# Optimization experiments

Measured on AMD Instinct MI355X. Metric: run time of the kernel, lower is better.

## Reference

```python
import jax, jax.numpy as jnp
import numpy as np

N = 100000; EI = 1600000; EC = 800000; G = 2000
FD = 512; H1 = 32; H2 = 32; EMB = 128; NH = 4
EPS = 1e-5


def setup_inputs() -> dict:
    key = jax.random.key(0)
    ks = jax.random.split(key, 30)
    p = lambda k, shp: (jax.random.normal(k, shp, jnp.float32) * 0.05)
    inp = {
        'feat': jax.random.normal(ks[0], (N, FD), jnp.float32),
        'inter_src': jax.random.randint(ks[1], (EI,), 0, N),
        'inter_dst': jax.random.randint(ks[2], (EI,), 0, N),
        'cross_src': jax.random.randint(ks[3], (EC,), 0, N),
        'cross_dst': jax.random.randint(ks[4], (EC,), 0, N),
        'graph_ids': jnp.sort(jax.random.randint(ks[5], (N,), 0, G)),
        # layer1
        'W_gc1': p(ks[6], (FD, NH * H1)), 'b_gc1': p(ks[7], (NH * H1,)),
        'W_gat1': p(ks[8], (FD, NH * H1)), 'al1': p(ks[9], (NH, H1)), 'ar1': p(ks[10], (NH, H1)), 'b_gat1': p(ks[11], (NH * H1,)),
        # layer2
        'W_gc2': p(ks[12], (NH * H1, NH * H2)), 'b_gc2': p(ks[13], (NH * H2,)),
        'W_gat2': p(ks[14], (NH * H1, NH * H2)), 'al2': p(ks[15], (NH, H2)), 'ar2': p(ks[16], (NH, H2)), 'b_gat2': p(ks[17], (NH * H2,)),
        # layer3
        'W_gc3': p(ks[18], (NH * H2, EMB)), 'b_gc3': p(ks[19], (EMB,)),
        'W_gat3': p(ks[20], (NH * H2, EMB)), 'al3': p(ks[21], (1, EMB)), 'ar3': p(ks[22], (1, EMB)), 'b_gat3': p(ks[23], (EMB,)),
        # batchnorms (gamma ones, beta zeros)
        'g1': jnp.ones((NH * H1,), jnp.float32), 'be1': jnp.zeros((NH * H1,), jnp.float32),
        'g2': jnp.ones((NH * H2,), jnp.float32), 'be2': jnp.zeros((NH * H2,), jnp.float32),
        'g3': jnp.ones((EMB,), jnp.float32), 'be3': jnp.zeros((EMB,), jnp.float32),
    }
    return inp


def _leaky(x):
    return jnp.where(x >= 0, x, 0.2 * x)


def _graph_conv(x, W, b, src, dst):
    # DGL GraphConv, norm='both': D_out^{-1/2} A D_in^{-1/2} X W + b (degrees clamped to >=1)
    ones = jnp.ones(src.shape[0], x.dtype)
    dout = jnp.clip(jax.ops.segment_sum(ones, src, num_segments=N), 1.0)
    din = jnp.clip(jax.ops.segment_sum(ones, dst, num_segments=N), 1.0)
    xw = (x @ W) * (dout ** -0.5)[:, None]          # project first (in >= out)
    agg = jax.ops.segment_sum(xw[src], dst, num_segments=N)
    return agg * (din ** -0.5)[:, None] + b


def _gat(x, W, al, ar, b, src, dst, H, d):
    # DGL GATConv: per-edge additive attention with edge softmax over incoming edges
    f = (x @ W).reshape(-1, H, d)                    # [N,H,d]
    el = jnp.sum(f * al, -1)                         # [N,H]
    er = jnp.sum(f * ar, -1)
    e = _leaky(el[src] + er[dst])                    # [E,H]
    m = jax.ops.segment_max(e, dst, num_segments=N)
    ex = jnp.exp(e - m[dst])
    s = jax.ops.segment_sum(ex, dst, num_segments=N)
    alpha = ex / s[dst]                              # [E,H]
    out = jax.ops.segment_sum(alpha[:, :, None] * f[src], dst, num_segments=N)
    return out + b.reshape(1, H, d), alpha


def _bn(x, g, b):
    mu = x.mean(0)
    v = jnp.mean((x - mu) ** 2, 0)
    return g * (x - mu) / jnp.sqrt(v + EPS) + b


def reference(feat, inter_src, inter_dst, cross_src, cross_dst, graph_ids,
              W_gc1, b_gc1, W_gat1, al1, ar1, b_gat1,
              W_gc2, b_gc2, W_gat2, al2, ar2, b_gat2,
              W_gc3, b_gc3, W_gat3, al3, ar3, b_gat3,
              g1, be1, g2, be2, g3, be3):
    h = feat
    hi = _graph_conv(h, W_gc1, b_gc1, inter_src, inter_dst)
    hc, _ = _gat(h, W_gat1, al1, ar1, b_gat1, cross_src, cross_dst, NH, H1)
    h = _bn(_leaky(hi + hc.reshape(N, -1)), g1, be1)
    hi = _graph_conv(h, W_gc2, b_gc2, inter_src, inter_dst)
    hc, _ = _gat(h, W_gat2, al2, ar2, b_gat2, cross_src, cross_dst, NH, H2)
    h = _bn(_leaky(hi + hc.reshape(N, -1)), g2, be2)
    h1 = _graph_conv(h, W_gc3, b_gc3, inter_src, inter_dst)
    h2, att = _gat(h, W_gat3, al3, ar3, b_gat3, cross_src, cross_dst, 1, EMB)
    h = _bn(h1 + h2[:, 0, :], g3, be3)
    att_sum = jax.ops.segment_sum(att[:, 0], cross_src, num_segments=N)   # [N]
    wh = h * att_sum[:, None]
    gsum = jax.ops.segment_sum(wh, graph_ids, num_segments=G)
    cnt = jnp.clip(jax.ops.segment_sum(jnp.ones(N, h.dtype), graph_ids, num_segments=G), 1.0)
    frag_embeddings = gsum / cnt[:, None]                                  # [G,EMB]
    return frag_embeddings, att_sum
```

## Files before the change

### kernel.cpp

```cpp
#include <hip/hip_runtime.h>
#include <math.h>

#define NN 100000
#define EIE 1600000
#define ECE 800000
#define GG 2000
#define FDIM 512
#define CC 128
#define BNEPS 1e-5f
#define SLOTI 48
#define SLOTC 32
#define FUSED_BLOCKS 3910

static inline int cdiv(long a, long b){ return (int)((a+b-1)/b); }

typedef __attribute__((ext_vector_type(8))) short short8;
typedef __attribute__((ext_vector_type(4))) float f32x4;

__device__ __forceinline__ unsigned short f2bf(float f){
  unsigned u = __float_as_uint(f);
  u += 0x7fffu + ((u >> 16) & 1u);
  return (unsigned short)(u >> 16);
}
__device__ __forceinline__ float bf2f(unsigned short h){
  return __uint_as_float(((unsigned)h) << 16);
}
__device__ __forceinline__ float2 ldbf2(const unsigned short* p){
  ushort2 u = *(const ushort2*)p;
  return make_float2(bf2f(u.x), bf2f(u.y));
}

__device__ __forceinline__ size_t wt_off(int n, int k) {
  return (size_t)(k >> 5)*8192 + (((n >> 4)*4 + ((k >> 3) & 3))*16 + (n & 15))*8 + (k & 7);
}
__global__ void k_pack_all(const float* __restrict__ Wgc1, const float* __restrict__ Wgat1,
                           const float* __restrict__ Wgc2, const float* __restrict__ Wgat2,
                           const float* __restrict__ Wgc3, const float* __restrict__ Wgat3,
                           unsigned short* __restrict__ Wth1, unsigned short* __restrict__ Wtl1,
                           unsigned short* __restrict__ Wth2, unsigned short* __restrict__ Wtl2,
                           unsigned short* __restrict__ Wth3, unsigned short* __restrict__ Wtl3) {
  int t = blockIdx.x*256 + threadIdx.x;
  const float *W1, *W2; unsigned short *oh, *ol; int FIN, tt;
  if (t < 131072)      { W1=Wgc1; W2=Wgat1; oh=Wth1; ol=Wtl1; FIN=512; tt=t; }
  else if (t < 163840) { W1=Wgc2; W2=Wgat2; oh=Wth2; ol=Wtl2; FIN=128; tt=t-131072; }
  else if (t < 196608) { W1=Wgc3; W2=Wgat3; oh=Wth3; ol=Wtl3; FIN=128; tt=t-163840; }
  else return;
  int n = tt / FIN, k = tt % FIN;
  float v = (n < 128) ? W1[(size_t)k*128 + n] : W2[(size_t)k*128 + (n-128)];
  unsigned short h = f2bf(v);
  size_t o = wt_off(n, k);
  oh[o] = h;
  ol[o] = f2bf(v - bf2f(h));
}

__global__ __launch_bounds__(512)
void k_fill_gemm1(const int* __restrict__ isrc, const int* __restrict__ idst,
                  const int* __restrict__ csrc, const int* __restrict__ cdst,
                  int* __restrict__ cnt_i, int* __restrict__ eid_i,
                  int* __restrict__ cnt_c, int* __restrict__ eid_c,
                  int* __restrict__ dout, float* __restrict__ att,
                  const float* __restrict__ xf,
                  const unsigned short* __restrict__ Bh, const unsigned short* __restrict__ Bl,
                  const float* __restrict__ al, const float* __restrict__ ar,
                  float* __restrict__ el, float* __restrict__ er,
                  unsigned short* __restrict__ Y1, unsigned short* __restrict__ Y2) {
  __shared__ __attribute__((aligned(16))) unsigned short sAh[4096];
  __shared__ __attribute__((aligned(16))) unsigned short sBh[8192];
  __shared__ __attribute__((aligned(16))) unsigned short sBl[8192];
  int r = blockIdx.x;
  int tid = threadIdx.x;

  if (r % 5 != 0) {
    int fi = r - 1 - (r-1)/5;
    int e = fi*512 + tid;
    if (e < EIE) {
      int d = idst[e];
      int p = atomicAdd(&cnt_i[d], 1);
      if (p < SLOTI) eid_i[d*SLOTI + p] = isrc[e];
      atomicAdd(&dout[isrc[e]], 1);
    }
    if (e < ECE) {
      int d = cdst[e];
      int p = atomicAdd(&cnt_c[d], 1);
      if (p < SLOTC) eid_c[d*SLOTC + p] = csrc[e];
    }
    if (e < NN) att[e] = 0.f;
    return;
  }

  int row0 = (r/5)*128;
  int lane = tid & 63, wid = tid >> 6;
  int wm = wid >> 2, wn = wid & 3;
  int l15 = lane & 15, quad = lane >> 4;

  f32x4 acc[4][4];
  #pragma unroll
  for (int mt = 0; mt < 4; ++mt)
    #pragma unroll
    for (int nt = 0; nt < 4; ++nt) acc[mt][nt] = (f32x4){0.f,0.f,0.f,0.f};

  for (int k0 = 0; k0 < FDIM; k0 += 32) {
    #pragma unroll
    for (int i = 0; i < 2; ++i) {
      int idx = tid + i*512;
      int rr = idx >> 3, c = idx & 7;
      int gr = row0 + rr; if (gr > NN-1) gr = NN-1;
      float4 v = *(const float4*)(xf + (size_t)gr*FDIM + k0 + c*4);
      ushort4 hh;
      hh.x = f2bf(v.x); hh.y = f2bf(v.y); hh.z = f2bf(v.z); hh.w = f2bf(v.w);
      *(ushort4*)&sAh[(((rr>>4)*4 + (c>>1))*16 + (rr&15))*8 + (c&1)*4] = hh;
    }
    const unsigned short* bhk = Bh + (size_t)k0*256;
    const unsigned short* blk = Bl + (size_t)k0*256;
    #pragma unroll
    for (int i = 0; i < 2; ++i) {
      int idx = tid + i*512;
      *(float4*)&sBh[idx*8] = *(const float4*)(bhk + idx*8);
      *(float4*)&sBl[idx*8] = *(const float4*)(blk + idx*8);
    }
    __syncthreads();
    short8 ah[4];
    #pragma unroll
    for (int mt = 0; mt < 4; ++mt)
      ah[mt] = *(const short8*)&sAh[(((wm*4+mt)*4 + quad)*16 + l15)*8];
    #pragma unroll
    for (int nt = 0; nt < 4; ++nt) {
      int off = (((wn*4+nt)*4 + quad)*16 + l15)*8;
      short8 bh = *(const short8*)&sBh[off];
      short8 bl = *(const short8*)&sBl[off];
      #pragma unroll
      for (int mt = 0; mt < 4; ++mt) {
        acc[mt][nt] = __builtin_amdgcn_mfma_f32_16x16x32_bf16(ah[mt], bh, acc[mt][nt], 0,0,0);
        acc[mt][nt] = __builtin_amdgcn_mfma_f32_16x16x32_bf16(ah[mt], bl, acc[mt][nt], 0,0,0);
      }
    }
    __syncthreads();
  }
  unsigned short* Y = (wn < 2) ? Y1 : Y2;
  int colbase = (wn & 1)*64;
  #pragma unroll
  for (int mt = 0; mt < 4; ++mt) {
    #pragma unroll
    for (int rr = 0; rr < 4; ++rr) {
      int row = row0 + (wm*4+mt)*16 + quad*4 + rr;
      if (row >= NN) continue;
      #pragma unroll
      for (int nt = 0; nt < 4; ++nt)
        Y[(size_t)row*CC + colbase + nt*16 + l15] = f2bf(acc[mt][nt][rr]);
    }
  }
  if (wn >= 2) {
    float alv[4], arv[4];
    #pragma unroll
    for (int nt = 0; nt < 4; ++nt) {
      int col = colbase + nt*16 + l15;
      alv[nt] = al[col]; arv[nt] = ar[col];
    }
    int hb = (wn & 1)*2;
    #pragma unroll
    for (int mt = 0; mt < 4; ++mt) {
      #pragma unroll
      for (int rr = 0; rr < 4; ++rr) {
        float pa0 = acc[mt][0][rr]*alv[0] + acc[mt][1][rr]*alv[1];
        float pb0 = acc[mt][0][rr]*arv[0] + acc[mt][1][rr]*arv[1];
        float pa1 = acc[mt][2][rr]*alv[2] + acc[mt][3][rr]*alv[3];
        float pb1 = acc[mt][2][rr]*arv[2] + acc[mt][3][rr]*arv[3];
        #pragma unroll
        for (int m = 1; m <= 8; m <<= 1) {
          pa0 += __shfl_xor(pa0, m); pb0 += __shfl_xor(pb0, m);
          pa1 += __shfl_xor(pa1, m); pb1 += __shfl_xor(pb1, m);
        }
        int row = row0 + (wm*4+mt)*16 + quad*4 + rr;
        if (l15 == 0 && row < NN) {
          el[(size_t)row*4 + hb]   = pa0;  er[(size_t)row*4 + hb]   = pb0;
          el[(size_t)row*4 + hb+1] = pa1;  er[(size_t)row*4 + hb+1] = pb1;
        }
      }
    }
  }
}

template<bool ELR4, bool ELR1>
__global__ __launch_bounds__(512)
void k_gemm2(const unsigned short* __restrict__ xb,
             const unsigned short* __restrict__ Bh, const unsigned short* __restrict__ Bl,
             const float* __restrict__ csqin, const float* __restrict__ g,
             const float* __restrict__ be, const int* __restrict__ dout,
             const float* __restrict__ al, const float* __restrict__ ar,
             float* __restrict__ el, float* __restrict__ er,
             unsigned short* __restrict__ Y1, unsigned short* __restrict__ Y2) {
  __shared__ __attribute__((aligned(16))) unsigned short sAh[4096];
  __shared__ __attribute__((aligned(16))) unsigned short sBh[8192];
  __shared__ __attribute__((aligned(16))) unsigned short sBl[8192];
  __shared__ float sSC[CC], sSH[CC];
  int tid = threadIdx.x;
  int row0 = blockIdx.x*128;
  int lane = tid & 63, wid = tid >> 6;
  int wm = wid >> 2, wn = wid & 3;
  int l15 = lane & 15, quad = lane >> 4;

  if (tid < CC) {
    float sv = csqin[tid], qv = csqin[CC + tid];
    float mu = sv * (1.f/NN);
    float var = qv * (1.f/NN) - mu*mu;
    float rn = rsqrtf(var + BNEPS);
    float s = g[tid]*rn;
    sSC[tid] = s;
    sSH[tid] = be[tid] - s*mu;
  }
  __syncthreads();

  f32x4 acc[4][4];
  #pragma unroll
  for (int mt = 0; mt < 4; ++mt)
    #pragma unroll
    for (int nt = 0; nt < 4; ++nt) acc[mt][nt] = (f32x4){0.f,0.f,0.f,0.f};

  for (int k0 = 0; k0 < CC; k0 += 32) {
    int rr = tid >> 2, c16 = tid & 3;
    int gr = row0 + rr; if (gr > NN-1) gr = NN-1;
    short8 u = *(const short8*)(xb + (size_t)gr*CC + k0 + c16*8);
    short8 o;
    #pragma unroll
    for (int j = 0; j < 8; ++j) {
      float f = bf2f((unsigned short)u[j]);
      f = f*sSC[k0 + c16*8 + j] + sSH[k0 + c16*8 + j];
      o[j] = (short)f2bf(f);
    }
    *(short8*)&sAh[(((rr>>4)*4 + c16)*16 + (rr&15))*8] = o;

    const unsigned short* bhk = Bh + (size_t)k0*256;
    const unsigned short* blk = Bl + (size_t)k0*256;
    #pragma unroll
    for (int i = 0; i < 2; ++i) {
      int idx = tid + i*512;
      *(float4*)&sBh[idx*8] = *(const float4*)(bhk + idx*8);
      *(float4*)&sBl[idx*8] = *(const float4*)(blk + idx*8);
    }
    __syncthreads();
    short8 ah[4];
    #pragma unroll
    for (int mt = 0; mt < 4; ++mt)
      ah[mt] = *(const short8*)&sAh[(((wm*4+mt)*4 + quad)*16 + l15)*8];
    #pragma unroll
    for (int nt = 0; nt < 4; ++nt) {
      int off = (((wn*4+nt)*4 + quad)*16 + l15)*8;
      short8 bh = *(const short8*)&sBh[off];
      short8 bl = *(const short8*)&sBl[off];
      #pragma unroll
      for (int mt = 0; mt < 4; ++mt) {
        acc[mt][nt] = __builtin_amdgcn_mfma_f32_16x16x32_bf16(ah[mt], bh, acc[mt][nt], 0,0,0);
        acc[mt][nt] = __builtin_amdgcn_mfma_f32_16x16x32_bf16(ah[mt], bl, acc[mt][nt], 0,0,0);
      }
    }
    __syncthreads();
  }
  unsigned short* Y = (wn < 2) ? Y1 : Y2;
  int colbase = (wn & 1)*64;
  #pragma unroll
  for (int mt = 0; mt < 4; ++mt) {
    #pragma unroll
    for (int rr = 0; rr < 4; ++rr) {
      int row = row0 + (wm*4+mt)*16 + quad*4 + rr;
      if (row >= NN) continue;
      float scv = (wn < 2) ? rsqrtf((float)max(dout[row], 1)) : 1.0f;
      #pragma unroll
      for (int nt = 0; nt < 4; ++nt)
        Y[(size_t)row*CC + colbase + nt*16 + l15] = f2bf(acc[mt][nt][rr]*scv);
    }
  }
  if constexpr (ELR4) {
    if (wn >= 2) {
      float alv[4], arv[4];
      #pragma unroll
      for (int nt = 0; nt < 4; ++nt) {
        int col = colbase + nt*16 + l15;
        alv[nt] = al[col]; arv[nt] = ar[col];
      }
      int hb = (wn & 1)*2;
      #pragma unroll
      for (int mt = 0; mt < 4; ++mt) {
        #pragma unroll
        for (int rr = 0; rr < 4; ++rr) {
          float pa0 = acc[mt][0][rr]*alv[0] + acc[mt][1][rr]*alv[1];
          float pb0 = acc[mt][0][rr]*arv[0] + acc[mt][1][rr]*arv[1];
          float pa1 = acc[mt][2][rr]*alv[2] + acc[mt][3][rr]*alv[3];
          float pb1 = acc[mt][2][rr]*arv[2] + acc[mt][3][rr]*arv[3];
          #pragma unroll
          for (int m = 1; m <= 8; m <<= 1) {
            pa0 += __shfl_xor(pa0, m); pb0 += __shfl_xor(pb0, m);
            pa1 += __shfl_xor(pa1, m); pb1 += __shfl_xor(pb1, m);
          }
          int row = row0 + (wm*4+mt)*16 + quad*4 + rr;
          if (l15 == 0 && row < NN) {
            el[(size_t)row*4 + hb]   = pa0;  er[(size_t)row*4 + hb]   = pb0;
            el[(size_t)row*4 + hb+1] = pa1;  er[(size_t)row*4 + hb+1] = pb1;
          }
        }
      }
    }
  }
  if constexpr (ELR1) {
    __shared__ float sE[2][2][CC];
    if (wn >= 2) {
      float alv[4], arv[4];
      #pragma unroll
      for (int nt = 0; nt < 4; ++nt) {
        int col = colbase + nt*16 + l15;
        alv[nt] = al[col]; arv[nt] = ar[col];
      }
      #pragma unroll
      for (int mt = 0; mt < 4; ++mt) {
        #pragma unroll
        for (int rr = 0; rr < 4; ++rr) {
          float pa = acc[mt][0][rr]*alv[0] + acc[mt][1][rr]*alv[1]
                   + acc[mt][2][rr]*alv[2] + acc[mt][3][rr]*alv[3];
          float pb = acc[mt][0][rr]*arv[0] + acc[mt][1][rr]*arv[1]
                   + acc[mt][2][rr]*arv[2] + acc[mt][3][rr]*arv[3];
          #pragma unroll
          for (int m = 1; m <= 8; m <<= 1) {
            pa += __shfl_xor(pa, m); pb += __shfl_xor(pb, m);
          }
          int rowl = (wm*4+mt)*16 + quad*4 + rr;
          if (l15 == 0) { sE[0][wn-2][rowl] = pa; sE[1][wn-2][rowl] = pb; }
        }
      }
    }
    __syncthreads();
    if (tid < CC) {
      int row = row0 + tid;
      if (row < NN) {
        el[row] = sE[0][0][tid] + sE[0][1][tid];
        er[row] = sE[1][0][tid] + sE[1][1][tid];
      }
    }
  }
}

template<int H, bool DSC, bool ATT, bool LEAKY>
__global__ __launch_bounds__(64)
void k_gather_fused(const unsigned short* __restrict__ A1, const unsigned short* __restrict__ A2,
                    const int* __restrict__ cnt_i, const int* __restrict__ eid_i,
                    const int* __restrict__ cnt_c, const int* __restrict__ eid_c,
                    const int* __restrict__ dout,
                    const float* __restrict__ el, const float* __restrict__ er,
                    const float* __restrict__ bgc, const float* __restrict__ bgat,
                    unsigned short* __restrict__ out, float* __restrict__ att) {
  int lane = threadIdx.x;
  int row = blockIdx.x;
  int grp = lane >> 4;
  int l4  = lane & 15;
  int c8  = l4*8;

  int deg = cnt_i[row];
  int lo = row*SLOTI, hi = lo + min(deg, SLOTI);
  float ax[8];
  #pragma unroll
  for (int k = 0; k < 8; ++k) ax[k] = 0.f;
  int j = lo + grp;
  for (; j + 4 < hi; j += 8) {
    int s0 = eid_i[j], s1 = eid_i[j+4];
    float d0 = DSC ? rsqrtf((float)max(dout[s0], 1)) : 1.0f;
    float d1 = DSC ? rsqrtf((float)max(dout[s1], 1)) : 1.0f;
    short8 u0 = *(const short8*)(A1 + (size_t)s0*CC + c8);
    short8 u1 = *(const short8*)(A1 + (size_t)s1*CC + c8);
    #pragma unroll
    for (int k = 0; k < 8; ++k) {
      if (DSC) ax[k] += d0*bf2f((unsigned short)u0[k]) + d1*bf2f((unsigned short)u1[k]);
      else     ax[k] += bf2f((unsigned short)u0[k]) + bf2f((unsigned short)u1[k]);
    }
  }
  if (j < hi) {
    int s0 = eid_i[j];
    float d0 = DSC ? rsqrtf((float)max(dout[s0], 1)) : 1.0f;
    short8 u0 = *(const short8*)(A1 + (size_t)s0*CC + c8);
    #pragma unroll
    for (int k = 0; k < 8; ++k) {
      if (DSC) ax[k] += d0*bf2f((unsigned short)u0[k]);
      else     ax[k] += bf2f((unsigned short)u0[k]);
    }
  }
  float sc = rsqrtf((float)max(deg, 1));

  int h = (H == 1) ? 0 : (l4 >> 2);
  float erd = er[(size_t)row*H + h];
  int degc = cnt_c[row];
  int lo2 = row*SLOTC, hi2 = lo2 + min(degc, SLOTC);
  float gacc[8];
  #pragma unroll
  for (int k = 0; k < 8; ++k) gacc[k] = 0.f;
  float denom = 0.f;
  j = lo2 + grp;
  for (; j + 4 < hi2; j += 8) {
    int s0 = eid_c[j], s1 = eid_c[j+4];
    float v0 = el[(size_t)s0*H + h] + erd;
    float v1 = el[(size_t)s1*H + h] + erd;
    v0 = (v0 >= 0.f) ? v0 : 0.2f*v0;
    v1 = (v1 >= 0.f) ? v1 : 0.2f*v1;
    float w0 = __expf(v0), w1 = __expf(v1);
    denom += w0 + w1;
    short8 u0 = *(const short8*)(A2 + (size_t)s0*CC + c8);
    short8 u1 = *(const short8*)(A2 + (size_t)s1*CC + c8);
    #pragma unroll
    for (int k = 0; k < 8; ++k)
      gacc[k] += w0*bf2f((unsigned short)u0[k]) + w1*bf2f((unsigned short)u1[k]);
  }
  if (j < hi2) {
    int s = eid_c[j];
    float v = el[(size_t)s*H + h] + erd;
    v = (v >= 0.f) ? v : 0.2f*v;
    float w = __expf(v);
    denom += w;
    short8 u = *(const short8*)(A2 + (size_t)s*CC + c8);
    #pragma unroll
    for (int k = 0; k < 8; ++k) gacc[k] += w * bf2f((unsigned short)u[k]);
  }

  #pragma unroll
  for (int m = 16; m <= 32; m <<= 1) {
    denom += __shfl_xor(denom, m);
    #pragma unroll
    for (int k = 0; k < 8; ++k) {
      ax[k]   += __shfl_xor(ax[k], m);
      gacc[k] += __shfl_xor(gacc[k], m);
    }
  }
  float inv = (denom > 0.f) ? 1.0f/denom : 0.f;

  if (ATT) {
    for (j = lo2 + grp; j < hi2; j += 4) {
      int s = eid_c[j];
      if (l4 == 0) {
        float v = el[(size_t)s*H] + erd;
        v = (v >= 0.f) ? v : 0.2f*v;
        atomicAdd(&att[s], __expf(v)*inv);
      }
    }
  }

  if (grp == 0) {
    float4 b1a = *(const float4*)(bgc + c8);
    float4 b1b = *(const float4*)(bgc + c8 + 4);
    float4 b2a = *(const float4*)(bgat + c8);
    float4 b2b = *(const float4*)(bgat + c8 + 4);
    float bb1[8] = {b1a.x,b1a.y,b1a.z,b1a.w,b1b.x,b1b.y,b1b.z,b1b.w};
    float bb2[8] = {b2a.x,b2a.y,b2a.z,b2a.w,b2b.x,b2b.y,b2b.z,b2b.w};
    short8 ov;
    #pragma unroll
    for (int k = 0; k < 8; ++k) {
      float o = ax[k]*sc + bb1[k] + gacc[k]*inv + bb2[k];
      if (LEAKY) o = (o >= 0.f) ? o : 0.2f*o;
      ov[k] = (short)f2bf(o);
    }
    *(short8*)(out + (size_t)row*CC + c8) = ov;
  }
}

__global__ __launch_bounds__(256)
void k_bn_stats(const unsigned short* __restrict__ t, float* __restrict__ csq) {
  __shared__ float red[4][128];
  int lane = threadIdx.x & 63, g = threadIdx.x >> 6;
  int c2 = lane*2;
  float s0=0.f, s1=0.f, q0=0.f, q1=0.f;
  for (int r = blockIdx.x*4 + g; r < NN; r += gridDim.x*4) {
    float2 v = ldbf2(t + (size_t)r*CC + c2);
    s0 += v.x; s1 += v.y; q0 += v.x*v.x; q1 += v.y*v.y;
  }
  red[g][c2] = s0; red[g][c2+1] = s1;
  __syncthreads();
  if (threadIdx.x < 128) {
    float a = red[0][threadIdx.x] + red[1][threadIdx.x] + red[2][threadIdx.x] + red[3][threadIdx.x];
    atomicAdd(&csq[threadIdx.x], a);
  }
  __syncthreads();
  red[g][c2] = q0; red[g][c2+1] = q1;
  __syncthreads();
  if (threadIdx.x < 128) {
    float a = red[0][threadIdx.x] + red[1][threadIdx.x] + red[2][threadIdx.x] + red[3][threadIdx.x];
    atomicAdd(&csq[128 + threadIdx.x], a);
  }
}

__global__ void k_bn_coef(const float* __restrict__ csqc,
                          const float* __restrict__ g, const float* __restrict__ be,
                          float* __restrict__ sc, float* __restrict__ sh) {
  int c = threadIdx.x;
  float mu = csqc[c] * (1.f/NN);
  float var = csqc[128+c] * (1.f/NN) - mu*mu;
  float r = rsqrtf(var + BNEPS);
  float s = g[c]*r;
  sc[c] = s;
  sh[c] = be[c] - s*mu;
}

__global__ void k_pool_bn(const unsigned short* __restrict__ t, const float* __restrict__ att,
                          const int* __restrict__ gids, const float* __restrict__ bnsc,
                          const float* __restrict__ bnsh, float* __restrict__ frag) {
  int g = blockIdx.x;
  __shared__ int se[2];
  if (threadIdx.x < 2) {
    int target = g + threadIdx.x;
    int lo = 0, hi = NN;
    while (lo < hi) { int mid = (lo + hi) >> 1; if (gids[mid] < target) lo = mid + 1; else hi = mid; }
    se[threadIdx.x] = lo;
  }
  __syncthreads();
  int lo = se[0], hi = se[1];
  int col = threadIdx.x;
  float scv = bnsc[col], shv = bnsh[col];
  float acc = 0.f;
  for (int n = lo; n < hi; ++n) acc += (bf2f(t[(size_t)n*CC + col])*scv + shv) * att[n];
  frag[(size_t)g*CC + col] = acc / (float)max(hi - lo, 1);
}

extern "C" void kernel_launch(void* const* d_in, const int* in_sizes, int n_in,
                              void* d_out, int out_size, void* d_ws, size_t ws_size,
                              hipStream_t stream) {
  const float* feat  = (const float*)d_in[0];
  const int* isrc    = (const int*)d_in[1];
  const int* idst    = (const int*)d_in[2];
  const int* csrc    = (const int*)d_in[3];
  const int* cdst    = (const int*)d_in[4];
  const int* gids    = (const int*)d_in[5];
  const float* W_gc1 = (const float*)d_in[6];  const float* b_gc1 = (const float*)d_in[7];
  const float* W_gat1= (const float*)d_in[8];  const float* al1   = (const float*)d_in[9];
  const float* ar1   = (const float*)d_in[10]; const float* b_gat1= (const float*)d_in[11];
  const float* W_gc2 = (const float*)d_in[12]; const float* b_gc2 = (const float*)d_in[13];
  const float* W_gat2= (const float*)d_in[14]; const float* al2   = (const float*)d_in[15];
  const float* ar2   = (const float*)d_in[16]; const float* b_gat2= (const float*)d_in[17];
  const float* W_gc3 = (const float*)d_in[18]; const float* b_gc3 = (const float*)d_in[19];
  const float* W_gat3= (const float*)d_in[20]; const float* al3   = (const float*)d_in[21];
  const float* ar3   = (const float*)d_in[22]; const float* b_gat3= (const float*)d_in[23];
  const float* g1 = (const float*)d_in[24]; const float* be1 = (const float*)d_in[25];
  const float* g2 = (const float*)d_in[26]; const float* be2 = (const float*)d_in[27];
  const float* g3 = (const float*)d_in[28]; const float* be3 = (const float*)d_in[29];

  const size_t NC = (size_t)NN*CC;
  float* el   = (float*)d_ws;
  float* er   = el + (size_t)NN*4;
  float* csq  = er + (size_t)NN*4;
  float* bnsc = csq + 768;
  float* bnsh = bnsc + CC;
  unsigned short* B  = (unsigned short*)(bnsh + CC);
  unsigned short* A1 = B + NC;
  unsigned short* A2 = A1 + NC;
  unsigned short* Wth1 = A2 + NC;
  unsigned short* Wtl1 = Wth1 + 256*FDIM;
  unsigned short* Wth2 = Wtl1 + 256*FDIM;
  unsigned short* Wtl2 = Wth2 + 256*CC;
  unsigned short* Wth3 = Wtl2 + 256*CC;
  unsigned short* Wtl3 = Wth3 + 256*CC;
  int* cnt_i  = (int*)(Wtl3 + 256*CC);
  int* cnt_c  = cnt_i + NN;
  int* dout   = cnt_c + NN;
  int* eid_i  = dout + NN;
  int* eid_c  = eid_i + (size_t)NN*SLOTI;

  float* frag = (float*)d_out;
  float* att  = frag + (size_t)GG*CC;

  hipMemsetAsync(cnt_i, 0, 3*(size_t)NN*sizeof(int), stream);
  hipMemsetAsync(csq, 0, 768*sizeof(float), stream);
  k_pack_all<<<cdiv(196608,256), 256, 0, stream>>>(W_gc1, W_gat1, W_gc2, W_gat2, W_gc3, W_gat3,
                                                   Wth1, Wtl1, Wth2, Wtl2, Wth3, Wtl3);
  k_fill_gemm1<<<FUSED_BLOCKS, 512, 0, stream>>>(isrc, idst, csrc, cdst,
                                                 cnt_i, eid_i, cnt_c, eid_c, dout, att,
                                                 feat, Wth1, Wtl1, al1, ar1, el, er, A1, A2);

  k_gather_fused<4,true,false,true><<<NN, 64, 0, stream>>>(A1, A2, cnt_i, eid_i,
                                                           cnt_c, eid_c, dout, el, er,
                                                           b_gc1, b_gat1, B, nullptr);
  k_bn_stats<<<256, 256, 0, stream>>>(B, csq);

  k_gemm2<true,false><<<cdiv(NN,128), 512, 0, stream>>>(B, Wth2, Wtl2, csq, g1, be1, dout,
                                                        al2, ar2, el, er, A1, A2);
  k_gather_fused<4,false,false,true><<<NN, 64, 0, stream>>>(A1, A2, cnt_i, eid_i,
                                                            cnt_c, eid_c, dout, el, er,
                                                            b_gc2, b_gat2, B, nullptr);
  k_bn_stats<<<256, 256, 0, stream>>>(B, csq + 256);

  k_gemm2<false,true><<<cdiv(NN,128), 512, 0, stream>>>(B, Wth3, Wtl3, csq + 256, g2, be2, dout,
                                                        al3, ar3, el, er, A1, A2);
  k_gather_fused<1,false,true,false><<<NN, 64, 0, stream>>>(A1, A2, cnt_i, eid_i,
                                                            cnt_c, eid_c, dout, el, er,
                                                            b_gc3, b_gat3, B, att);
  k_bn_stats<<<256, 256, 0, stream>>>(B, csq + 512);
  k_bn_coef<<<1, 128, 0, stream>>>(csq + 512, g3, be3, bnsc, bnsh);

  k_pool_bn<<<GG, 128, 0, stream>>>(B, att, gids, bnsc, bnsh, frag);
}
```

Baseline: 997.7 us.

## Fuse batchnorm statistics into persistent gather kernel with per-wave partials

The gather kernel becomes a grid-stride persistent kernel: 8192 waves, two per 128-thread block, each loop over many rows. Each wave accumulates per-channel sum and sum of squares of its fp32 outputs and writes them to a partials buffer. A small reduction kernel then folds the partials into the stats buffer, replacing the separate pass that re-read the bf16 output. This removes one full read of the activations per layer and the per-row block launch overhead, but adds a partials buffer and computes stats on pre-rounding fp32 values rather than the stored bf16 ones.

```diff
diff --git a/kernel.cpp b/kernel.cpp
--- a/kernel.cpp
+++ b/kernel.cpp
@@ -11,6 +11,8 @@
 #define SLOTI 48
 #define SLOTC 32
 #define FUSED_BLOCKS 3910
+#define GWG 4096
+#define NWAVES 8192
 
 static inline int cdiv(long a, long b){ return (int)((a+b-1)/b); }
 
@@ -338,147 +340,152 @@
 }
 
 template<int H, bool DSC, bool ATT, bool LEAKY>
-__global__ __launch_bounds__(64)
+__global__ __launch_bounds__(128)
 void k_gather_fused(const unsigned short* __restrict__ A1, const unsigned short* __restrict__ A2,
                     const int* __restrict__ cnt_i, const int* __restrict__ eid_i,
                     const int* __restrict__ cnt_c, const int* __restrict__ eid_c,
                     const int* __restrict__ dout,
                     const float* __restrict__ el, const float* __restrict__ er,
                     const float* __restrict__ bgc, const float* __restrict__ bgat,
-                    unsigned short* __restrict__ out, float* __restrict__ att) {
-  int lane = threadIdx.x;
-  int row = blockIdx.x;
+                    unsigned short* __restrict__ out, float* __restrict__ att,
+                    float* __restrict__ partial) {
+  int lane = threadIdx.x & 63;
+  int wave = blockIdx.x*2 + (threadIdx.x >> 6);
   int grp = lane >> 4;
   int l4  = lane & 15;
   int c8  = l4*8;
 
-  int deg = cnt_i[row];
-  int lo = row*SLOTI, hi = lo + min(deg, SLOTI);
-  float ax[8];
-  #pragma unroll
-  for (int k = 0; k < 8; ++k) ax[k] = 0.f;
-  int j = lo + grp;
-  for (; j + 4 < hi; j += 8) {
-    int s0 = eid_i[j], s1 = eid_i[j+4];
-    float d0 = DSC ? rsqrtf((float)max(dout[s0], 1)) : 1.0f;
-    float d1 = DSC ? rsqrtf((float)max(dout[s1], 1)) : 1.0f;
-    short8 u0 = *(const short8*)(A1 + (size_t)s0*CC + c8);
-    short8 u1 = *(const short8*)(A1 + (size_t)s1*CC + c8);
+  float bb1[8], bb2[8];
+  {
+    float4 a = *(const float4*)(bgc + c8);
+    float4 b = *(const float4*)(bgc + c8 + 4);
+    float4 c = *(const float4*)(bgat + c8);
+    float4 d = *(const float4*)(bgat + c8 + 4);
+    bb1[0]=a.x; bb1[1]=a.y; bb1[2]=a.z; bb1[3]=a.w;
+    bb1[4]=b.x; bb1[5]=b.y; bb1[6]=b.z; bb1[7]=b.w;
+    bb2[0]=c.x; bb2[1]=c.y; bb2[2]=c.z; bb2[3]=c.w;
+    bb2[4]=d.x; bb2[5]=d.y; bb2[6]=d.z; bb2[7]=d.w;
+  }
+  float s2x = 0.f, s2y = 0.f, q2x = 0.f, q2y = 0.f;
+
+  for (int row = wave; row < NN; row += NWAVES) {
+    int deg = cnt_i[row];
+    int lo = row*SLOTI, hi = lo + min(deg, SLOTI);
+    float ax[8];
+    #pragma unroll
+    for (int k = 0; k < 8; ++k) ax[k] = 0.f;
+    int j = lo + grp;
+    for (; j + 4 < hi; j += 8) {
+      int s0 = eid_i[j], s1 = eid_i[j+4];
+      float d0 = DSC ? rsqrtf((float)max(dout[s0], 1)) : 1.0f;
+      float d1 = DSC ? rsqrtf((float)max(dout[s1], 1)) : 1.0f;
+      short8 u0 = *(const short8*)(A1 + (size_t)s0*CC + c8);
+      short8 u1 = *(const short8*)(A1 + (size_t)s1*CC + c8);
+      #pragma unroll
+      for (int k = 0; k < 8; ++k) {
+        if (DSC) ax[k] += d0*bf2f((unsigned short)u0[k]) + d1*bf2f((unsigned short)u1[k]);
+        else     ax[k] += bf2f((unsigned short)u0[k]) + bf2f((unsigned short)u1[k]);
+      }
+    }
+    if (j < hi) {
+      int s0 = eid_i[j];
+      float d0 = DSC ? rsqrtf((float)max(dout[s0], 1)) : 1.0f;
+      short8 u0 = *(const short8*)(A1 + (size_t)s0*CC + c8);
+      #pragma unroll
+      for (int k = 0; k < 8; ++k) {
+        if (DSC) ax[k] += d0*bf2f((unsigned short)u0[k]);
+        else     ax[k] += bf2f((unsigned short)u0[k]);
+      }
+    }
+    float sc = rsqrtf((float)max(deg, 1));
+
+    int h = (H == 1) ? 0 : (l4 >> 2);
+    float erd = er[(size_t)row*H + h];
+    int degc = cnt_c[row];
+    int lo2 = row*SLOTC, hi2 = lo2 + min(degc, SLOTC);
+    float gacc[8];
+    #pragma unroll
+    for (int k = 0; k < 8; ++k) gacc[k] = 0.f;
+    float denom = 0.f;
+    j = lo2 + grp;
+    for (; j + 4 < hi2; j += 8) {
+      int s0 = eid_c[j], s1 = eid_c[j+4];
+      float v0 = el[(size_t)s0*H + h] + erd;
+      float v1 = el[(size_t)s1*H + h] + erd;
+      v0 = (v0 >= 0.f) ? v0 : 0.2f*v0;
+      v1 = (v1 >= 0.f) ? v1 : 0.2f*v1;
+      float w0 = __expf(v0), w1 = __expf(v1);
+      denom += w0 + w1;
+      short8 u0 = *(const short8*)(A2 + (size_t)s0*CC + c8);
+      short8 u1 = *(const short8*)(A2 + (size_t)s1*CC + c8);
+      #pragma unroll
+      for (int k = 0; k < 8; ++k)
+        gacc[k] += w0*bf2f((unsigned short)u0[k]) + w1*bf2f((unsigned short)u1[k]);
+    }
+    if (j < hi2) {
+      int s = eid_c[j];
+      float v = el[(size_t)s*H + h] + erd;
+      v = (v >= 0.f) ? v : 0.2f*v;
+      float w = __expf(v);
+      denom += w;
+      short8 u = *(const short8*)(A2 + (size_t)s*CC + c8);
+      #pragma unroll
+      for (int k = 0; k < 8; ++k) gacc[k] += w * bf2f((unsigned short)u[k]);
+    }
+
+    #pragma unroll
+    for (int m = 16; m <= 32; m <<= 1) {
+      denom += __shfl_xor(denom, m);
+      #pragma unroll
+      for (int k = 0; k < 8; ++k) {
+        ax[k]   += __shfl_xor(ax[k], m);
+        gacc[k] += __shfl_xor(gacc[k], m);
+      }
+    }
+    float inv = (denom > 0.f) ? 1.0f/denom : 0.f;
+
+    if (ATT) {
+      for (j = lo2 + grp; j < hi2; j += 4) {
+        int s = eid_c[j];
+        if (l4 == 0) {
+          float v = el[(size_t)s*H] + erd;
+          v = (v >= 0.f) ? v : 0.2f*v;
+          atomicAdd(&att[s], __expf(v)*inv);
+        }
+      }
+    }
+
+    float o[8];
     #pragma unroll
     for (int k = 0; k < 8; ++k) {
-      if (DSC) ax[k] += d0*bf2f((unsigned short)u0[k]) + d1*bf2f((unsigned short)u1[k]);
-      else     ax[k] += bf2f((unsigned short)u0[k]) + bf2f((unsigned short)u1[k]);
-    }
-  }
-  if (j < hi) {
-    int s0 = eid_i[j];
-    float d0 = DSC ? rsqrtf((float)max(dout[s0], 1)) : 1.0f;
-    short8 u0 = *(const short8*)(A1 + (size_t)s0*CC + c8);
-    #pragma unroll
-    for (int k = 0; k < 8; ++k) {
-      if (DSC) ax[k] += d0*bf2f((unsigned short)u0[k]);
-      else     ax[k] += bf2f((unsigned short)u0[k]);
-    }
-  }
-  float sc = rsqrtf((float)max(deg, 1));
-
-  int h = (H == 1) ? 0 : (l4 >> 2);
-  float erd = er[(size_t)row*H + h];
-  int degc = cnt_c[row];
-  int lo2 = row*SLOTC, hi2 = lo2 + min(degc, SLOTC);
-  float gacc[8];
-  #pragma unroll
-  for (int k = 0; k < 8; ++k) gacc[k] = 0.f;
-  float denom = 0.f;
-  j = lo2 + grp;
-  for (; j + 4 < hi2; j += 8) {
-    int s0 = eid_c[j], s1 = eid_c[j+4];
-    float v0 = el[(size_t)s0*H + h] + erd;
-    float v1 = el[(size_t)s1*H + h] + erd;
-    v0 = (v0 >= 0.f) ? v0 : 0.2f*v0;
-    v1 = (v1 >= 0.f) ? v1 : 0.2f*v1;
-    float w0 = __expf(v0), w1 = __expf(v1);
-    denom += w0 + w1;
-    short8 u0 = *(const short8*)(A2 + (size_t)s0*CC + c8);
-    short8 u1 = *(const short8*)(A2 + (size_t)s1*CC + c8);
-    #pragma unroll
-    for (int k = 0; k < 8; ++k)
-      gacc[k] += w0*bf2f((unsigned short)u0[k]) + w1*bf2f((unsigned short)u1[k]);
-  }
-  if (j < hi2) {
-    int s = eid_c[j];
-    float v = el[(size_t)s*H + h] + erd;
-    v = (v >= 0.f) ? v : 0.2f*v;
-    float w = __expf(v);
-    denom += w;
-    short8 u = *(const short8*)(A2 + (size_t)s*CC + c8);
-    #pragma unroll
-    for (int k = 0; k < 8; ++k) gacc[k] += w * bf2f((unsigned short)u[k]);
-  }
-
-  #pragma unroll
-  for (int m = 16; m <= 32; m <<= 1) {
-    denom += __shfl_xor(denom, m);
-    #pragma unroll
-    for (int k = 0; k < 8; ++k) {
-      ax[k]   += __shfl_xor(ax[k], m);
-      gacc[k] += __shfl_xor(gacc[k], m);
-    }
-  }
-  float inv = (denom > 0.f) ? 1.0f/denom : 0.f;
-
-  if (ATT) {
-    for (j = lo2 + grp; j < hi2; j += 4) {
-      int s = eid_c[j];
-      if (l4 == 0) {
-        float v = el[(size_t)s*H] + erd;
-        v = (v >= 0.f) ? v : 0.2f*v;
-        atomicAdd(&att[s], __expf(v)*inv);
-      }
-    }
-  }
-
-  if (grp == 0) {
-    float4 b1a = *(const float4*)(bgc + c8);
-    float4 b1b = *(const float4*)(bgc + c8 + 4);
-    float4 b2a = *(const float4*)(bgat + c8);
-    float4 b2b = *(const float4*)(bgat + c8 + 4);
-    float bb1[8] = {b1a.x,b1a.y,b1a.z,b1a.w,b1b.x,b1b.y,b1b.z,b1b.w};
-    float bb2[8] = {b2a.x,b2a.y,b2a.z,b2a.w,b2b.x,b2b.y,b2b.z,b2b.w};
-    short8 ov;
-    #pragma unroll
-    for (int k = 0; k < 8; ++k) {
-      float o = ax[k]*sc + bb1[k] + gacc[k]*inv + bb2[k];
-      if (LEAKY) o = (o >= 0.f) ? o : 0.2f*o;
-      ov[k] = (short)f2bf(o);
-    }
-    *(short8*)(out + (size_t)row*CC + c8) = ov;
-  }
+      float v = ax[k]*sc + bb1[k] + gacc[k]*inv + bb2[k];
+      if (LEAKY) v = (v >= 0.f) ? v : 0.2f*v;
+      o[k] = v;
+    }
+    if (grp == 0) {
+      short8 ov;
+      #pragma unroll
+      for (int k = 0; k < 8; ++k) ov[k] = (short)f2bf(o[k]);
+      *(short8*)(out + (size_t)row*CC + c8) = ov;
+    }
+    float ox = o[2*grp], oy = o[2*grp+1];
+    s2x += ox; s2y += oy;
+    q2x += ox*ox; q2y += oy*oy;
+  }
+
+  float* p = partial + (size_t)wave*256;
+  *(float2*)(p + c8 + 2*grp)       = make_float2(s2x, s2y);
+  *(float2*)(p + 128 + c8 + 2*grp) = make_float2(q2x, q2y);
 }
 
 __global__ __launch_bounds__(256)
-void k_bn_stats(const unsigned short* __restrict__ t, float* __restrict__ csq) {
-  __shared__ float red[4][128];
-  int lane = threadIdx.x & 63, g = threadIdx.x >> 6;
-  int c2 = lane*2;
-  float s0=0.f, s1=0.f, q0=0.f, q1=0.f;
-  for (int r = blockIdx.x*4 + g; r < NN; r += gridDim.x*4) {
-    float2 v = ldbf2(t + (size_t)r*CC + c2);
-    s0 += v.x; s1 += v.y; q0 += v.x*v.x; q1 += v.y*v.y;
-  }
-  red[g][c2] = s0; red[g][c2+1] = s1;
-  __syncthreads();
-  if (threadIdx.x < 128) {
-    float a = red[0][threadIdx.x] + red[1][threadIdx.x] + red[2][threadIdx.x] + red[3][threadIdx.x];
-    atomicAdd(&csq[threadIdx.x], a);
-  }
-  __syncthreads();
-  red[g][c2] = q0; red[g][c2+1] = q1;
-  __syncthreads();
-  if (threadIdx.x < 128) {
-    float a = red[0][threadIdx.x] + red[1][threadIdx.x] + red[2][threadIdx.x] + red[3][threadIdx.x];
-    atomicAdd(&csq[128 + threadIdx.x], a);
-  }
+void k_bn_red(const float* __restrict__ partial, float* __restrict__ csq) {
+  int t = threadIdx.x;
+  float a = 0.f;
+  int w0 = blockIdx.x*256;
+  for (int w = w0; w < w0 + 256; ++w)
+    a += partial[(size_t)w*256 + t];
+  atomicAdd(&csq[t], a);
 }
 
 __global__ void k_bn_coef(const float* __restrict__ csqc,
@@ -555,6 +562,7 @@
   int* dout   = cnt_c + NN;
   int* eid_i  = dout + NN;
   int* eid_c  = eid_i + (size_t)NN*SLOTI;
+  float* partial = (float*)(eid_c + (size_t)NN*SLOTC);
 
   float* frag = (float*)d_out;
   float* att  = frag + (size_t)GG*CC;
@@ -567,24 +575,24 @@
                                                  cnt_i, eid_i, cnt_c, eid_c, dout, att,
                                                  feat, Wth1, Wtl1, al1, ar1, el, er, A1, A2);
 
-  k_gather_fused<4,true,false,true><<<NN, 64, 0, stream>>>(A1, A2, cnt_i, eid_i,
-                                                           cnt_c, eid_c, dout, el, er,
-                                                           b_gc1, b_gat1, B, nullptr);
-  k_bn_stats<<<256, 256, 0, stream>>>(B, csq);
+  k_gather_fused<4,true,false,true><<<GWG, 128, 0, stream>>>(A1, A2, cnt_i, eid_i,
+                                                             cnt_c, eid_c, dout, el, er,
+                                                             b_gc1, b_gat1, B, nullptr, partial);
+  k_bn_red<<<NWAVES/256, 256, 0, stream>>>(partial, csq);
 
   k_gemm2<true,false><<<cdiv(NN,128), 512, 0, stream>>>(B, Wth2, Wtl2, csq, g1, be1, dout,
                                                         al2, ar2, el, er, A1, A2);
-  k_gather_fused<4,false,false,true><<<NN, 64, 0, stream>>>(A1, A2, cnt_i, eid_i,
-                                                            cnt_c, eid_c, dout, el, er,
-                                                            b_gc2, b_gat2, B, nullptr);
-  k_bn_stats<<<256, 256, 0, stream>>>(B, csq + 256);
+  k_gather_fused<4,false,false,true><<<GWG, 128, 0, stream>>>(A1, A2, cnt_i, eid_i,
+                                                              cnt_c, eid_c, dout, el, er,
+                                                              b_gc2, b_gat2, B, nullptr, partial);
+  k_bn_red<<<NWAVES/256, 256, 0, stream>>>(partial, csq + 256);
 
   k_gemm2<false,true><<<cdiv(NN,128), 512, 0, stream>>>(B, Wth3, Wtl3, csq + 256, g2, be2, dout,
                                                         al3, ar3, el, er, A1, A2);
-  k_gather_fused<1,false,true,false><<<NN, 64, 0, stream>>>(A1, A2, cnt_i, eid_i,
-                                                            cnt_c, eid_c, dout, el, er,
-                                                            b_gc3, b_gat3, B, att);
-  k_bn_stats<<<256, 256, 0, stream>>>(B, csq + 512);
+  k_gather_fused<1,false,true,false><<<GWG, 128, 0, stream>>>(A1, A2, cnt_i, eid_i,
+                                                              cnt_c, eid_c, dout, el, er,
+                                                              b_gc3, b_gat3, B, att, partial);
+  k_bn_red<<<NWAVES/256, 256, 0, stream>>>(partial, csq + 512);
   k_bn_coef<<<1, 128, 0, stream>>>(csq + 512, g3, be3, bnsc, bnsh);
 
   k_pool_bn<<<GG, 128, 0, stream>>>(B, att, gids, bnsc, bnsh, frag);
```

Measured after the change: 1.075 ms. +7.8%, slower.
